# Kernel optimization log

Measured on AMD Instinct MI355X. Metric: run time of the kernel, lower is better.

The kernel has to match this reference:

```python
import jax, jax.numpy as jnp
import numpy as np

B, N, RESC, LAT, UNIT = 8, 32, 256.0, 1536, 512
CHS = [64, 64, 128, 256, 512, 512]
HS = [128, 64, 32, 16, 8, 1]


def _align(feat, P):
    # torch F.grid_sample(feat, 2*P.unsqueeze(-2)/RESC - 1, 'bilinear', 'border', align_corners=False).squeeze(-1)
    # feat: [B,C,H,W], P: [B,M,2] (x,y) pixel coords in [0,RESC); returns [B,C,M]
    Bn, C, H, W = feat.shape
    gx = 2.0 * P[..., 0] / RESC - 1.0
    gy = 2.0 * P[..., 1] / RESC - 1.0
    # align_corners=False unnormalize, then border clamp
    x = jnp.clip(((gx + 1.0) * W - 1.0) * 0.5, 0.0, W - 1.0)
    y = jnp.clip(((gy + 1.0) * H - 1.0) * 0.5, 0.0, H - 1.0)
    x0 = jnp.floor(x); y0 = jnp.floor(y)
    wx = (x - x0)[:, None, :]; wy = (y - y0)[:, None, :]
    x0i = x0.astype(jnp.int32); y0i = y0.astype(jnp.int32)
    x1i = jnp.minimum(x0i + 1, W - 1); y1i = jnp.minimum(y0i + 1, H - 1)
    flat = feat.reshape(Bn, C, H * W)
    def gat(yi, xi):
        return jnp.take_along_axis(flat, (yi * W + xi)[:, None, :], axis=2)  # [B,C,M]
    v00 = gat(y0i, x0i); v01 = gat(y0i, x1i); v10 = gat(y1i, x0i); v11 = gat(y1i, x1i)
    return v00 * (1 - wx) * (1 - wy) + v01 * wx * (1 - wy) + v10 * (1 - wx) * wy + v11 * wx * wy


def _conv1(x, w, b):
    # 1x1 Conv1d: [B,Cin,M] x [Cout,Cin] -> [B,Cout,M]
    return jnp.einsum('bci,oc->boi', x, w) + b[None, :, None]


def _rescls(x, p):
    # ResCls(n=1): intro -> (relu(BN) -> chorus, residual) -> outro ; BN in eval mode
    iw, ib, bg, bb, bm, bv, cw, cb, ow, ob = p
    x = _conv1(x, iw, ib)
    d = jax.nn.relu((x - bm[None, :, None]) * (bg / jnp.sqrt(bv + 1e-5))[None, :, None] + bb[None, :, None])
    x = x + _conv1(d, cw, cb)
    return _conv1(x, ow, ob)


def _forward(feats, P, n, gp, pp):
    # node features: concat of per-level aligned features  [B, LAT, N]
    F_ = jnp.concatenate([_align(f, P) for f in feats], axis=1)
    # edge midpoints ep[b, i*N+j] = (P[i] + P[j]) / 2  -> [B, N*N, 2]
    ep = ((P[:, :, None, :] + P[:, None, :, :]) * 0.5).reshape(B, N * N, 2)
    # L: first LAT channels = F[:, :, i], next LAT channels = F[:, :, j]
    Fi = jnp.broadcast_to(F_[:, :, :, None], (B, LAT, N, N)).reshape(B, LAT, N * N)
    Fj = jnp.broadcast_to(F_[:, :, None, :], (B, LAT, N, N)).reshape(B, LAT, N * N)
    E = jnp.concatenate([_align(f, ep) for f in feats], axis=1)  # [B, LAT, N*N]
    CE = jnp.concatenate([Fi, Fj, E], axis=1)  # [B, 3*LAT, N*N]
    gate = jax.nn.sigmoid(_rescls(CE, gp))  # [B, 1, N*N]
    pr = _rescls(CE, pp)  # [B, 64, N*N]
    pr = pr / jnp.maximum(jnp.linalg.norm(pr, axis=1, keepdims=True), 1e-12)  # F.normalize(dim=1)
    m = jnp.arange(N) < n[:, None]  # [B, N]
    mask = (m[:, None, :] & m[:, :, None]).reshape(B, 1, N * N).astype(CE.dtype)
    return (gate * pr * mask).reshape(B, 64, N, N)


def setup_inputs() -> dict:
    key = jax.random.key(0)
    ks = jax.random.split(key, 20)
    d = {}
    for i, (c, h) in enumerate(zip(CHS, HS)):
        d[f'feat{i}'] = jax.random.normal(ks[i], (B, c, h, h), jnp.float32)
    d['P'] = jax.random.uniform(ks[6], (B, N, 2), jnp.float32) * RESC
    d['n'] = jax.random.randint(ks[7], (B,), 16, N + 1, jnp.int32)
    def w(k, shape):
        return jax.random.normal(k, shape, jnp.float32) * 0.02
    for pre, cout, k0 in (('g', 1, 8), ('p', 64, 12)):
        d[pre + '_iw'] = w(ks[k0], (UNIT, 3 * LAT)); d[pre + '_ib'] = jnp.zeros((UNIT,), jnp.float32)
        d[pre + '_bg'] = jnp.ones((UNIT,), jnp.float32); d[pre + '_bb'] = jnp.zeros((UNIT,), jnp.float32)
        d[pre + '_bm'] = jnp.zeros((UNIT,), jnp.float32)
        d[pre + '_bv'] = jax.random.uniform(ks[k0 + 1], (UNIT,), jnp.float32) + 0.5
        d[pre + '_cw'] = w(ks[k0 + 2], (UNIT, UNIT)); d[pre + '_cb'] = jnp.zeros((UNIT,), jnp.float32)
        d[pre + '_ow'] = w(ks[k0 + 3], (cout, UNIT)); d[pre + '_ob'] = jnp.zeros((cout,), jnp.float32)
    return d


def reference(feat0, feat1, feat2, feat3, feat4, feat5, P, n,
              g_iw, g_ib, g_bg, g_bb, g_bm, g_bv, g_cw, g_cb, g_ow, g_ob,
              p_iw, p_ib, p_bg, p_bb, p_bm, p_bv, p_cw, p_cb, p_ow, p_ob):
    feats = (feat0, feat1, feat2, feat3, feat4, feat5)
    gp = (g_iw, g_ib, g_bg, g_bb, g_bm, g_bv, g_cw, g_cb, g_ow, g_ob)
    pp = (p_iw, p_ib, p_bg, p_bb, p_bm, p_bv, p_cw, p_cb, p_ow, p_ob)
    return _forward(feats, P, n, gp, pp)
```

## Files before the change

### kernel.cpp

```cpp
#include <hip/hip_runtime.h>
#include <hip/hip_bf16.h>

using bf16 = __hip_bfloat16;
using short8 = __attribute__((ext_vector_type(8))) short;
using f32x4  = __attribute__((ext_vector_type(4))) float;
typedef unsigned int u32;

#define LAT_ 1536

__device__ __forceinline__ void glds16(const bf16* g, bf16* l) {
  __builtin_amdgcn_global_load_lds(
      (const __attribute__((address_space(1))) void*)g,
      (__attribute__((address_space(3))) void*)l, 16, 0, 0);
}
__device__ __forceinline__ float b2f(bf16 x) { return __bfloat162float(x); }
__device__ __forceinline__ bf16 f2b(float x) { return __float2bfloat16(x); }

template<int C, int W>
__device__ __forceinline__ void trans_tile(const float* __restrict__ src, bf16* __restrict__ dst,
                                           int b, int hw0, int c0, bf16 (*tile)[72], int t) {
  constexpr int HW = W * W;
  {
    int cl = t >> 2, h0 = (t & 3) * 16;
    const float* sp = src + (long)(b * C + c0 + cl) * HW + hw0 + h0;
    #pragma unroll
    for (int k = 0; k < 16; k += 4) {
      float4 v = *(const float4*)(sp + k);
      tile[h0 + k + 0][cl] = f2b(v.x);
      tile[h0 + k + 1][cl] = f2b(v.y);
      tile[h0 + k + 2][cl] = f2b(v.z);
      tile[h0 + k + 3][cl] = f2b(v.w);
    }
  }
  __syncthreads();
  {
    int hwl = t >> 2, cc = (t & 3) * 16;
    bf16* dp = dst + ((long)b * HW + hw0 + hwl) * C + c0 + cc;
    #pragma unroll
    for (int k = 0; k < 16; k += 2) {
      __hip_bfloat162 pr;
      pr.x = tile[hwl][cc + k];
      pr.y = tile[hwl][cc + k + 1];
      *(__hip_bfloat162*)(dp + k) = pr;
    }
  }
}

__global__ __launch_bounds__(256) void prep_k(
    const float* __restrict__ g_iw, const float* __restrict__ p_iw,
    const float* __restrict__ p_cw, const float* __restrict__ p_ow, const float* __restrict__ f5,
    const float* __restrict__ g_bg, const float* __restrict__ g_bb, const float* __restrict__ g_bm,
    const float* __restrict__ g_bv, const float* __restrict__ p_bg, const float* __restrict__ p_bb,
    const float* __restrict__ p_bm, const float* __restrict__ p_bv,
    const float* __restrict__ g_ib, const float* __restrict__ p_ib, const float* __restrict__ p_cb,
    const float* __restrict__ g_ow, const float* __restrict__ g_cw,
    const float* __restrict__ g_cb, const float* __restrict__ g_ob,
    const float* __restrict__ f0, const float* __restrict__ f1, const float* __restrict__ f2,
    const float* __restrict__ f3, const float* __restrict__ f4,
    bf16* __restrict__ Wp, bf16* __restrict__ pcw16, bf16* __restrict__ pow16,
    bf16* __restrict__ T5, float* __restrict__ bnp, float* __restrict__ u,
    float* __restrict__ gacc,
    bf16* __restrict__ T0, bf16* __restrict__ T1, bf16* __restrict__ T2,
    bf16* __restrict__ T3, bf16* __restrict__ T4) {
  __shared__ bf16 tile[64][72];
  __shared__ float red[256];
  int B = blockIdx.x, t = threadIdx.x;
  if (B < 18432) {
    int seg = B / 3072;
    int idx = (B % 3072) * 256 + t;
    if (idx < 512 * 1536) {
      int r = idx / 1536, c = idx % 1536;
      const float* src; int co;
      switch (seg) {
        case 0: src = g_iw; co = 0;    break;
        case 1: src = g_iw; co = 1536; break;
        case 2: src = p_iw; co = 0;    break;
        case 3: src = p_iw; co = 1536; break;
        case 4: src = g_iw; co = 3072; break;
        default: src = p_iw; co = 3072; break;
      }
      Wp[(long)seg * 512 * 1536 + idx] = f2b(src[(long)r * 4608 + co + c]);
    }
    return;
  }
  if (B < 19456) { int idx = (B - 18432) * 256 + t; pcw16[idx] = f2b(p_cw[idx]); return; }
  if (B < 19584) { int idx = (B - 19456) * 256 + t; pow16[idx] = f2b(p_ow[idx]); return; }
  if (B < 19600) { int idx = (B - 19584) * 256 + t; T5[idx] = f2b(f5[idx]); return; }
  if (B < 19602) {
    int k = (B - 19600) * 256 + t;
    if (k < 512) {
      float sg = g_bg[k] / sqrtf(g_bv[k] + 1e-5f);
      bnp[k] = sg; bnp[512 + k] = g_bb[k] - g_bm[k] * sg;
      float sp = p_bg[k] / sqrtf(p_bv[k] + 1e-5f);
      bnp[1024 + k] = sp; bnp[1536 + k] = p_bb[k] - p_bm[k] * sp;
      bnp[2048 + k] = g_ib[k]; bnp[2560 + k] = p_ib[k];
      bnp[3584 + k] = p_cb[k];
    }
    return;
  }
  if (B < 19610) {
    __shared__ float ured[4][64];
    int k0 = (B - 19602) * 64;
    int kk = t & 63, part = t >> 6;
    int k = k0 + kk;
    float s = 0.f;
    for (int o = part * 128; o < part * 128 + 128; ++o)
      s = fmaf(g_ow[o], g_cw[o * 512 + k], s);
    ured[part][kk] = s;
    __syncthreads();
    if (part == 0) u[k] = ured[0][kk] + ured[1][kk] + ured[2][kk] + ured[3][kk];
    return;
  }
  if (B == 19610) {
    red[t] = g_ow[t] * g_cb[t] + g_ow[t + 256] * g_cb[t + 256];
    __syncthreads();
    for (int off = 128; off; off >>= 1) {
      if (t < off) red[t] += red[t + off];
      __syncthreads();
    }
    if (t == 0) bnp[3072] = red[0] + g_ob[0];
    return;
  }
  if (B < 19643) { int idx = (B - 19611) * 256 + t; gacc[idx] = 0.f; return; }
  {
    int q = B - 19643;
    int b = q / 376, tt = q % 376;
    if (tt < 256)      trans_tile<64, 128>(f0, T0, b, tt * 64, 0, tile, t);
    else if (tt < 320) trans_tile<64, 64 >(f1, T1, b, (tt - 256) * 64, 0, tile, t);
    else if (tt < 352) { int z = tt - 320; trans_tile<128, 32>(f2, T2, b, (z & 15) * 64, (z >> 4) * 64, tile, t); }
    else if (tt < 368) { int z = tt - 352; trans_tile<256, 16>(f3, T3, b, (z & 3) * 64, (z >> 2) * 64, tile, t); }
    else               { int z = tt - 368; trans_tile<512, 8 >(f4, T4, b, 0, z * 64, tile, t); }
  }
}

__device__ __forceinline__ float blo(u32 r) { return __uint_as_float(r << 16); }
__device__ __forceinline__ float bhi(u32 r) { return __uint_as_float(r & 0xffff0000u); }

template<int C, int W>
__device__ __forceinline__ void proc2(const bf16* __restrict__ T, int b,
    const float* MX, const float* MY, bf16* __restrict__ Sb, int koff, int t) {
  constexpr int C2 = C / 2, HW = W * W;
  const bf16* Tb = T + (long)b * HW * C;
  for (int idx = t; idx < 16 * C2; idx += 256) {
    int q = idx / C2, c2 = idx % C2;
    float x = MX[q], y = MY[q];
    float fx = fminf(fmaxf(x * ((float)W / 256.f) - 0.5f, 0.f), (float)(W - 1));
    float fy = fminf(fmaxf(y * ((float)W / 256.f) - 0.5f, 0.f), (float)(W - 1));
    float x0f = floorf(fx), y0f = floorf(fy);
    float wx = fx - x0f, wy = fy - y0f;
    int x0 = (int)x0f, y0 = (int)y0f;
    int x1 = min(x0 + 1, W - 1), y1 = min(y0 + 1, W - 1);
    u32 r00 = *(const u32*)&Tb[(y0 * W + x0) * C + 2 * c2];
    u32 r01 = *(const u32*)&Tb[(y0 * W + x1) * C + 2 * c2];
    u32 r10 = *(const u32*)&Tb[(y1 * W + x0) * C + 2 * c2];
    u32 r11 = *(const u32*)&Tb[(y1 * W + x1) * C + 2 * c2];
    float w00 = (1.f - wx) * (1.f - wy), w01 = wx * (1.f - wy);
    float w10 = (1.f - wx) * wy,        w11 = wx * wy;
    float vlo = blo(r00) * w00 + blo(r01) * w01 + blo(r10) * w10 + blo(r11) * w11;
    float vhi = bhi(r00) * w00 + bhi(r01) * w01 + bhi(r10) * w10 + bhi(r11) * w11;
    __hip_bfloat162 pr;
    pr.x = f2b(vlo); pr.y = f2b(vhi);
    *(__hip_bfloat162*)&Sb[(long)q * LAT_ + koff + 2 * c2] = pr;
  }
}

__global__ __launch_bounds__(256) void sample5_k(
    const bf16* __restrict__ T0, const bf16* __restrict__ T1, const bf16* __restrict__ T2,
    const bf16* __restrict__ T3, const bf16* __restrict__ T4, const bf16* __restrict__ T5,
    const float* __restrict__ P, bf16* __restrict__ Sball) {
  int b = blockIdx.z, p0 = blockIdx.x * 16, lvl = blockIdx.y, t = threadIdx.x;
  __shared__ float Px[32], Py[32], MX[16], MY[16];
  if (t < 32) { Px[t] = P[(b * 32 + t) * 2]; Py[t] = P[(b * 32 + t) * 2 + 1]; }
  __syncthreads();
  if (t < 16) {
    int m = p0 + t;
    float x, y;
    if (m < 32) { x = Px[m]; y = Py[m]; }
    else { int ij = m - 32, i = ij >> 5, j = ij & 31;
           x = 0.5f * (Px[i] + Px[j]); y = 0.5f * (Py[i] + Py[j]); }
    MX[t] = x; MY[t] = y;
  }
  __syncthreads();
  bf16* Sb = Sball + ((long)b * 1056 + p0) * LAT_;
  switch (lvl) {
    case 0: proc2<64, 128>(T0, b, MX, MY, Sb, 0,    t); break;
    case 1: proc2<64, 64 >(T1, b, MX, MY, Sb, 64,   t); break;
    case 2: proc2<128, 32>(T2, b, MX, MY, Sb, 128,  t); break;
    case 3: proc2<256, 16>(T3, b, MX, MY, Sb, 256,  t); break;
    case 4: proc2<512, 8 >(T4, b, MX, MY, Sb, 512,  t); break;
    default:
      for (int idx = t; idx < 16 * 256; idx += 256) {
        int q = idx >> 8, c2 = idx & 255;
        *(__hip_bfloat162*)&Sb[(long)q * LAT_ + 1024 + 2 * c2] =
            *(const __hip_bfloat162*)&T5[b * 512 + 2 * c2];
      }
  }
}

__global__ __launch_bounds__(256) void nodegemm_k(
    const bf16* __restrict__ Sball, const bf16* __restrict__ Wp, float* __restrict__ A4) {
  int b = blockIdx.y;
  int n0 = blockIdx.x * 64;
  int t = threadIdx.x, w = t >> 6, lane = t & 63;
  int nn = n0 + w * 16;
  int frow = lane & 15, fko = (lane >> 4) * 8;
  const bf16* Ab = Sball + (long)b * 1056 * LAT_;
  f32x4 acc[2] = {};
  for (int kb = 0; kb < LAT_; kb += 32) {
    short8 bq = *(const short8*)&Wp[(long)(nn + frow) * LAT_ + kb + fko];
    #pragma unroll
    for (int i = 0; i < 2; ++i) {
      short8 aq = *(const short8*)&Ab[(long)(i * 16 + frow) * LAT_ + kb + fko];
      acc[i] = __builtin_amdgcn_mfma_f32_16x16x32_bf16(aq, bq, acc[i], 0, 0, 0);
    }
  }
  #pragma unroll
  for (int i = 0; i < 2; ++i)
    #pragma unroll
    for (int r = 0; r < 4; ++r) {
      int m = i * 16 + (lane >> 4) * 4 + r;
      int n = nn + (lane & 15);
      A4[(long)b * 65536 + m * 2048 + n] = acc[i][r];
    }
}

__global__ __launch_bounds__(256) void edge_k(
    const bf16* __restrict__ Sball, const bf16* __restrict__ WpE,
    const float* __restrict__ bnp, const float* __restrict__ A4,
    const float* __restrict__ u, const float* __restrict__ g_ow,
    bf16* __restrict__ XFh, bf16* __restrict__ DH, float* __restrict__ gacc) {
  int b = blockIdx.z;
  int m0 = blockIdx.x * 128, n0 = blockIdx.y * 128;
  const bf16* A = Sball + (long)b * 1056 * LAT_ + 32 * LAT_;
  __shared__ bf16 Ash[128 * 32];
  __shared__ bf16 Bsh[128 * 32];
  int t = threadIdx.x, w = t >> 6, lane = t & 63;
  int mh = (w & 1) * 64, nh = (w >> 1) * 64;
  int frow = lane & 15, fko = (lane >> 4) * 8;
  int lrow = lane >> 2, lchunk = lane & 3;
  f32x4 acc[4][4] = {};
  for (int kb = 0; kb < LAT_; kb += 32) {
    #pragma unroll
    for (int q = 0; q < 2; ++q) {
      int ra = q * 64 + w * 16 + lrow;
      glds16(&A[(long)(m0 + ra) * LAT_ + kb + lchunk * 8],   &Ash[ra * 32 + lchunk * 8]);
      glds16(&WpE[(long)(n0 + ra) * LAT_ + kb + lchunk * 8], &Bsh[ra * 32 + lchunk * 8]);
    }
    __syncthreads();
    short8 af[4], bq[4];
    #pragma unroll
    for (int i = 0; i < 4; ++i) af[i] = *(const short8*)&Ash[(mh + i * 16 + frow) * 32 + fko];
    #pragma unroll
    for (int j = 0; j < 4; ++j) bq[j] = *(const short8*)&Bsh[(nh + j * 16 + frow) * 32 + fko];
    #pragma unroll
    for (int i = 0; i < 4; ++i)
      #pragma unroll
      for (int j = 0; j < 4; ++j)
        acc[i][j] = __builtin_amdgcn_mfma_f32_16x16x32_bf16(af[i], bq[j], acc[i][j], 0, 0, 0);
    __syncthreads();
  }
  if (n0 < 512) {
    float pg[16];
    #pragma unroll
    for (int z = 0; z < 16; ++z) pg[z] = 0.f;
    #pragma unroll
    for (int i = 0; i < 4; ++i) {
      #pragma unroll
      for (int j = 0; j < 4; ++j) {
        int n = n0 + nh + j * 16 + (lane & 15);
        float gw = g_ow[n], uu = u[n];
        float sc = bnp[n], sh = bnp[512 + n], ib = bnp[2048 + n];
        #pragma unroll
        for (int r = 0; r < 4; ++r) {
          int m = m0 + mh + i * 16 + (lane >> 4) * 4 + r;
          float v = acc[i][j][r] + ib
                  + A4[((long)b * 32 + (m >> 5)) * 2048 + n]
                  + A4[((long)b * 32 + (m & 31)) * 2048 + 512 + n];
          float d = fmaxf(fmaf(v, sc, sh), 0.f);
          pg[i * 4 + r] += gw * v + uu * d;
        }
      }
    }
    #pragma unroll
    for (int z = 0; z < 16; ++z) {
      float v = pg[z];
      v += __shfl_xor(v, 1, 16);
      v += __shfl_xor(v, 2, 16);
      v += __shfl_xor(v, 4, 16);
      v += __shfl_xor(v, 8, 16);
      pg[z] = v;
    }
    if ((lane & 15) == 0) {
      #pragma unroll
      for (int z = 0; z < 16; ++z) {
        int m = m0 + mh + (z >> 2) * 16 + (lane >> 4) * 4 + (z & 3);
        atomicAdd(&gacc[(long)b * 1024 + m], pg[z]);
      }
    }
  } else {
    #pragma unroll
    for (int i = 0; i < 4; ++i) {
      #pragma unroll
      for (int j = 0; j < 4; ++j) {
        int n = n0 + nh + j * 16 + (lane & 15);
        int np = n - 512;
        float sc = bnp[1024 + np], sh = bnp[1536 + np], ib = bnp[2048 + n];
        #pragma unroll
        for (int r = 0; r < 4; ++r) {
          int m = m0 + mh + i * 16 + (lane >> 4) * 4 + r;
          float v = acc[i][j][r] + ib
                  + A4[((long)b * 32 + (m >> 5)) * 2048 + 1024 + np]
                  + A4[((long)b * 32 + (m & 31)) * 2048 + 1536 + np];
          long e = ((long)b * 1024 + m) * 512 + np;
          XFh[e] = f2b(v);
          DH[e]  = f2b(fmaxf(fmaf(v, sc, sh), 0.f));
        }
      }
    }
  }
}

__global__ __launch_bounds__(256) void chorus_k(
    const bf16* __restrict__ DH, const bf16* __restrict__ pcw16,
    const float* __restrict__ bnp, const bf16* __restrict__ XFh,
    bf16* __restrict__ Yp16) {
  int b = blockIdx.z;
  int m0 = blockIdx.x * 128, n0 = blockIdx.y * 128;
  const bf16* A = DH + (long)b * 1024 * 512;
  __shared__ bf16 Ash[128 * 32];
  __shared__ bf16 Bsh[128 * 32];
  int t = threadIdx.x, w = t >> 6, lane = t & 63;
  int mh = (w & 1) * 64, nh = (w >> 1) * 64;
  int frow = lane & 15, fko = (lane >> 4) * 8;
  int lrow = lane >> 2, lchunk = lane & 3;
  f32x4 acc[4][4] = {};
  for (int kb = 0; kb < 512; kb += 32) {
    #pragma unroll
    for (int q = 0; q < 2; ++q) {
      int ra = q * 64 + w * 16 + lrow;
      glds16(&A[(long)(m0 + ra) * 512 + kb + lchunk * 8],      &Ash[ra * 32 + lchunk * 8]);
      glds16(&pcw16[(long)(n0 + ra) * 512 + kb + lchunk * 8],  &Bsh[ra * 32 + lchunk * 8]);
    }
    __syncthreads();
    short8 af[4], bq[4];
    #pragma unroll
    for (int i = 0; i < 4; ++i) af[i] = *(const short8*)&Ash[(mh + i * 16 + frow) * 32 + fko];
    #pragma unroll
    for (int j = 0; j < 4; ++j) bq[j] = *(const short8*)&Bsh[(nh + j * 16 + frow) * 32 + fko];
    #pragma unroll
    for (int i = 0; i < 4; ++i)
      #pragma unroll
      for (int j = 0; j < 4; ++j)
        acc[i][j] = __builtin_amdgcn_mfma_f32_16x16x32_bf16(af[i], bq[j], acc[i][j], 0, 0, 0);
    __syncthreads();
  }
  #pragma unroll
  for (int i = 0; i < 4; ++i)
    #pragma unroll
    for (int j = 0; j < 4; ++j)
      #pragma unroll
      for (int r = 0; r < 4; ++r) {
        int m = m0 + mh + i * 16 + (lane >> 4) * 4 + r;
        int n = n0 + nh + j * 16 + (lane & 15);
        float v = acc[i][j][r] + bnp[3584 + n]
                + b2f(XFh[((long)b * 1024 + m) * 512 + n]);
        Yp16[((long)b * 1024 + m) * 512 + n] = f2b(v);
      }
}

__global__ __launch_bounds__(256) void ofinal_k(
    const bf16* __restrict__ Yp16, const bf16* __restrict__ pow16,
    const float* __restrict__ p_ob, const float* __restrict__ gacc,
    const float* __restrict__ bnp, const int* __restrict__ nvec,
    float* __restrict__ out) {
  int b = blockIdx.y;
  int m0 = blockIdx.x * 64;
  const bf16* Ab = Yp16 + (long)b * 1024 * 512;
  __shared__ bf16 Ash[64][40];
  __shared__ bf16 Bsh[64][40];
  __shared__ float ol[64][65];
  int t = threadIdx.x, w = t >> 6, lane = t & 63;
  int mq = w * 16;
  int frow = lane & 15, fko = (lane >> 4) * 8;
  f32x4 acc[4] = {};
  for (int kb = 0; kb < 512; kb += 32) {
    { int r = t >> 2, ko = (t & 3) * 8;
      *(uint4*)&Ash[r][ko] = *(const uint4*)&Ab[(long)(m0 + r) * 512 + kb + ko];
      *(uint4*)&Bsh[r][ko] = *(const uint4*)&pow16[(long)r * 512 + kb + ko]; }
    __syncthreads();
    short8 af = *(const short8*)&Ash[mq + frow][fko];
    #pragma unroll
    for (int j = 0; j < 4; ++j) {
      short8 bq = *(const short8*)&Bsh[j * 16 + frow][fko];
      acc[j] = __builtin_amdgcn_mfma_f32_16x16x32_bf16(af, bq, acc[j], 0, 0, 0);
    }
    __syncthreads();
  }
  float pr[4][4], ssl[4] = {0.f, 0.f, 0.f, 0.f};
  #pragma unroll
  for (int j = 0; j < 4; ++j) {
    float bias = p_ob[j * 16 + (lane & 15)];
    #pragma unroll
    for (int r = 0; r < 4; ++r) {
      float v = acc[j][r] + bias;
      pr[j][r] = v;
      ssl[r] = fmaf(v, v, ssl[r]);
    }
  }
  #pragma unroll
  for (int r = 0; r < 4; ++r) {
    float v = ssl[r];
    v += __shfl_xor(v, 1, 16);
    v += __shfl_xor(v, 2, 16);
    v += __shfl_xor(v, 4, 16);
    v += __shfl_xor(v, 8, 16);
    ssl[r] = v;
  }
  int nb = nvec[b];
  float gconst = bnp[3072];
  float scale[4];
  #pragma unroll
  for (int r = 0; r < 4; ++r) {
    int m = m0 + mq + (lane >> 4) * 4 + r;
    float gl = gacc[(long)b * 1024 + m] + gconst;
    float gate = 1.f / (1.f + expf(-gl));
    int ii = m >> 5, jj = m & 31;
    float maskv = (ii < nb && jj < nb) ? 1.f : 0.f;
    scale[r] = gate * maskv / fmaxf(sqrtf(ssl[r]), 1e-12f);
  }
  #pragma unroll
  for (int j = 0; j < 4; ++j)
    #pragma unroll
    for (int r = 0; r < 4; ++r)
      ol[mq + (lane >> 4) * 4 + r][j * 16 + (lane & 15)] = pr[j][r] * scale[r];
  __syncthreads();
  {
    int c = t >> 2, ms = (t & 3) * 16;
    float* op = out + ((long)b * 64 + c) * 1024 + m0 + ms;
    #pragma unroll
    for (int k = 0; k < 16; k += 4) {
      float4 v;
      v.x = ol[ms + k + 0][c];
      v.y = ol[ms + k + 1][c];
      v.z = ol[ms + k + 2][c];
      v.w = ol[ms + k + 3][c];
      *(float4*)(op + k) = v;
    }
  }
}

extern "C" void kernel_launch(void* const* d_in, const int* in_sizes, int n_in,
                              void* d_out, int out_size, void* d_ws, size_t ws_size,
                              hipStream_t stream) {
  const float* f0 = (const float*)d_in[0];
  const float* f1 = (const float*)d_in[1];
  const float* f2 = (const float*)d_in[2];
  const float* f3 = (const float*)d_in[3];
  const float* f4 = (const float*)d_in[4];
  const float* f5 = (const float*)d_in[5];
  const float* P  = (const float*)d_in[6];
  const int*   n  = (const int*)d_in[7];
  const float *g_iw=(const float*)d_in[8],  *g_ib=(const float*)d_in[9],
              *g_bg=(const float*)d_in[10], *g_bb=(const float*)d_in[11],
              *g_bm=(const float*)d_in[12], *g_bv=(const float*)d_in[13],
              *g_cw=(const float*)d_in[14], *g_cb=(const float*)d_in[15],
              *g_ow=(const float*)d_in[16], *g_ob=(const float*)d_in[17];
  const float *p_iw=(const float*)d_in[18], *p_ib=(const float*)d_in[19],
              *p_bg=(const float*)d_in[20], *p_bb=(const float*)d_in[21],
              *p_bm=(const float*)d_in[22], *p_bv=(const float*)d_in[23],
              *p_cw=(const float*)d_in[24], *p_cb=(const float*)d_in[25],
              *p_ow=(const float*)d_in[26], *p_ob=(const float*)d_in[27];
  float* out = (float*)d_out;
  char* wsb = (char*)d_ws;

  bf16*  Sb    = (bf16*)(wsb + 0);
  bf16*  Wp    = (bf16*)(wsb + 25952256);
  bf16*  pcw16 = (bf16*)(wsb + 35389440);
  bf16*  pow16 = (bf16*)(wsb + 35913728);
  bf16*  T5    = (bf16*)(wsb + 35979264);
  float* bnp   = (float*)(wsb + 35987456);
  float* u     = (float*)(wsb + 36003840);
  float* gacc  = (float*)(wsb + 36005888);
  float* A4    = (float*)(wsb + 36038656);
  bf16*  XFh   = (bf16*)(wsb + 38135808);
  bf16*  DH    = (bf16*)(wsb + 46524416);
  bf16*  Yp16  = (bf16*)(wsb + 54913024);
  bf16*  T0 = (bf16*)(wsb + 38135808);
  bf16*  T1 = (bf16*)(wsb + 54913024);
  bf16*  T2 = (bf16*)(wsb + 59107328);
  bf16*  T3 = (bf16*)(wsb + 61204480);
  bf16*  T4 = (bf16*)(wsb + 62253056);
  bf16*  WpE = Wp + (long)2048 * LAT_;

  prep_k<<<22651, 256, 0, stream>>>(g_iw, p_iw, p_cw, p_ow, f5,
      g_bg, g_bb, g_bm, g_bv, p_bg, p_bb, p_bm, p_bv, g_ib, p_ib, p_cb,
      g_ow, g_cw, g_cb, g_ob, f0, f1, f2, f3, f4,
      Wp, pcw16, pow16, T5, bnp, u, gacc, T0, T1, T2, T3, T4);
  sample5_k<<<dim3(66, 6, 8), 256, 0, stream>>>(T0, T1, T2, T3, T4, T5, P, Sb);
  nodegemm_k<<<dim3(32, 8), 256, 0, stream>>>(Sb, Wp, A4);
  edge_k<<<dim3(8, 8, 8), 256, 0, stream>>>(Sb, WpE, bnp, A4, u, g_ow, XFh, DH, gacc);
  chorus_k<<<dim3(8, 4, 8), 256, 0, stream>>>(DH, pcw16, bnp, XFh, Yp16);
  ofinal_k<<<dim3(16, 8), 256, 0, stream>>>(Yp16, pow16, p_ob, gacc, bnp, n, out);
}
```

Measured before the change: 256.8 us.

## Fold chorus conv into output conv and merge tail kernels into one

Precomputes V = p_ow·p_cw and a folded bias in the prep kernel. This lets the final output be computed as XF·p_owᵀ + DH·Vᵀ in one fused post kernel, replacing the separate 512-wide chorus GEMM and the output GEMM, along with their bf16 intermediate round-trip. The node GEMM is also restructured so each block loops over all 8 batches while reusing the weight fragment, which leaves 32 blocks instead of 256. The risks are bf16 rounding of the folded V, a naive serial 512-length dot product per element in prep, and reduced parallelism in the node GEMM.

```diff
diff --git a/kernel.cpp b/kernel.cpp
--- a/kernel.cpp
+++ b/kernel.cpp
@@ -53,11 +53,12 @@
     const float* __restrict__ g_bv, const float* __restrict__ p_bg, const float* __restrict__ p_bb,
     const float* __restrict__ p_bm, const float* __restrict__ p_bv,
     const float* __restrict__ g_ib, const float* __restrict__ p_ib, const float* __restrict__ p_cb,
+    const float* __restrict__ p_ob,
     const float* __restrict__ g_ow, const float* __restrict__ g_cw,
     const float* __restrict__ g_cb, const float* __restrict__ g_ob,
     const float* __restrict__ f0, const float* __restrict__ f1, const float* __restrict__ f2,
     const float* __restrict__ f3, const float* __restrict__ f4,
-    bf16* __restrict__ Wp, bf16* __restrict__ pcw16, bf16* __restrict__ pow16,
+    bf16* __restrict__ Wp, bf16* __restrict__ pow16, bf16* __restrict__ V16,
     bf16* __restrict__ T5, float* __restrict__ bnp, float* __restrict__ u,
     float* __restrict__ gacc,
     bf16* __restrict__ T0, bf16* __restrict__ T1, bf16* __restrict__ T2,
@@ -83,24 +84,22 @@
     }
     return;
   }
-  if (B < 19456) { int idx = (B - 18432) * 256 + t; pcw16[idx] = f2b(p_cw[idx]); return; }
-  if (B < 19584) { int idx = (B - 19456) * 256 + t; pow16[idx] = f2b(p_ow[idx]); return; }
-  if (B < 19600) { int idx = (B - 19584) * 256 + t; T5[idx] = f2b(f5[idx]); return; }
-  if (B < 19602) {
-    int k = (B - 19600) * 256 + t;
+  if (B < 18560) { int idx = (B - 18432) * 256 + t; pow16[idx] = f2b(p_ow[idx]); return; }
+  if (B < 18576) { int idx = (B - 18560) * 256 + t; T5[idx] = f2b(f5[idx]); return; }
+  if (B < 18578) {
+    int k = (B - 18576) * 256 + t;
     if (k < 512) {
       float sg = g_bg[k] / sqrtf(g_bv[k] + 1e-5f);
       bnp[k] = sg; bnp[512 + k] = g_bb[k] - g_bm[k] * sg;
       float sp = p_bg[k] / sqrtf(p_bv[k] + 1e-5f);
       bnp[1024 + k] = sp; bnp[1536 + k] = p_bb[k] - p_bm[k] * sp;
       bnp[2048 + k] = g_ib[k]; bnp[2560 + k] = p_ib[k];
-      bnp[3584 + k] = p_cb[k];
     }
     return;
   }
-  if (B < 19610) {
+  if (B < 18586) {
     __shared__ float ured[4][64];
-    int k0 = (B - 19602) * 64;
+    int k0 = (B - 18578) * 64;
     int kk = t & 63, part = t >> 6;
     int k = k0 + kk;
     float s = 0.f;
@@ -111,7 +110,7 @@
     if (part == 0) u[k] = ured[0][kk] + ured[1][kk] + ured[2][kk] + ured[3][kk];
     return;
   }
-  if (B == 19610) {
+  if (B == 18586) {
     red[t] = g_ow[t] * g_cb[t] + g_ow[t + 256] * g_cb[t + 256];
     __syncthreads();
     for (int off = 128; off; off >>= 1) {
@@ -121,9 +120,26 @@
     if (t == 0) bnp[3072] = red[0] + g_ob[0];
     return;
   }
-  if (B < 19643) { int idx = (B - 19611) * 256 + t; gacc[idx] = 0.f; return; }
+  if (B < 18619) { int idx = (B - 18587) * 256 + t; gacc[idx] = 0.f; return; }
+  if (B < 18747) {
+    int idx = (B - 18619) * 256 + t;
+    int c = idx >> 9, k = idx & 511;
+    float s = 0.f;
+    for (int nn = 0; nn < 512; ++nn)
+      s = fmaf(p_ow[c * 512 + nn], p_cw[nn * 512 + k], s);
+    V16[idx] = f2b(s);
+    return;
+  }
+  if (B == 18747) {
+    if (t < 64) {
+      float s = p_ob[t];
+      for (int nn = 0; nn < 512; ++nn) s = fmaf(p_ow[t * 512 + nn], p_cb[nn], s);
+      bnp[3104 + t] = s;
+    }
+    return;
+  }
   {
-    int q = B - 19643;
+    int q = B - 18748;
     int b = q / 376, tt = q % 376;
     if (tt < 256)      trans_tile<64, 128>(f0, T0, b, tt * 64, 0, tile, t);
     else if (tt < 320) trans_tile<64, 64 >(f1, T1, b, (tt - 256) * 64, 0, tile, t);
@@ -199,29 +215,33 @@
 
 __global__ __launch_bounds__(256) void nodegemm_k(
     const bf16* __restrict__ Sball, const bf16* __restrict__ Wp, float* __restrict__ A4) {
-  int b = blockIdx.y;
   int n0 = blockIdx.x * 64;
   int t = threadIdx.x, w = t >> 6, lane = t & 63;
   int nn = n0 + w * 16;
   int frow = lane & 15, fko = (lane >> 4) * 8;
-  const bf16* Ab = Sball + (long)b * 1056 * LAT_;
-  f32x4 acc[2] = {};
+  f32x4 acc[8][2] = {};
   for (int kb = 0; kb < LAT_; kb += 32) {
     short8 bq = *(const short8*)&Wp[(long)(nn + frow) * LAT_ + kb + fko];
     #pragma unroll
-    for (int i = 0; i < 2; ++i) {
-      short8 aq = *(const short8*)&Ab[(long)(i * 16 + frow) * LAT_ + kb + fko];
-      acc[i] = __builtin_amdgcn_mfma_f32_16x16x32_bf16(aq, bq, acc[i], 0, 0, 0);
+    for (int b = 0; b < 8; ++b) {
+      const bf16* Ab = Sball + (long)b * 1056 * LAT_;
+      #pragma unroll
+      for (int i = 0; i < 2; ++i) {
+        short8 aq = *(const short8*)&Ab[(long)(i * 16 + frow) * LAT_ + kb + fko];
+        acc[b][i] = __builtin_amdgcn_mfma_f32_16x16x32_bf16(aq, bq, acc[b][i], 0, 0, 0);
+      }
     }
   }
   #pragma unroll
-  for (int i = 0; i < 2; ++i)
-    #pragma unroll
-    for (int r = 0; r < 4; ++r) {
-      int m = i * 16 + (lane >> 4) * 4 + r;
-      int n = nn + (lane & 15);
-      A4[(long)b * 65536 + m * 2048 + n] = acc[i][r];
-    }
+  for (int b = 0; b < 8; ++b)
+    #pragma unroll
+    for (int i = 0; i < 2; ++i)
+      #pragma unroll
+      for (int r = 0; r < 4; ++r) {
+        int m = i * 16 + (lane >> 4) * 4 + r;
+        int n = nn + (lane & 15);
+        A4[(long)b * 65536 + m * 2048 + n] = acc[b][i][r];
+      }
 }
 
 __global__ __launch_bounds__(256) void edge_k(
@@ -320,125 +340,114 @@
   }
 }
 
-__global__ __launch_bounds__(256) void chorus_k(
-    const bf16* __restrict__ DH, const bf16* __restrict__ pcw16,
-    const float* __restrict__ bnp, const bf16* __restrict__ XFh,
-    bf16* __restrict__ Yp16) {
-  int b = blockIdx.z;
-  int m0 = blockIdx.x * 128, n0 = blockIdx.y * 128;
-  const bf16* A = DH + (long)b * 1024 * 512;
-  __shared__ bf16 Ash[128 * 32];
-  __shared__ bf16 Bsh[128 * 32];
+__global__ __launch_bounds__(256) void post_k(
+    const bf16* __restrict__ XFh, const bf16* __restrict__ DH,
+    const bf16* __restrict__ pow16, const bf16* __restrict__ V16,
+    const float* __restrict__ bnp, const float* __restrict__ gacc,
+    const int* __restrict__ nvec, float* __restrict__ out) {
+  int b = blockIdx.y;
+  int m0 = blockIdx.x * 128;
+  __shared__ float smem_f[128 * 65];
+  bf16* Xsh = (bf16*)smem_f;
+  bf16* Dsh = Xsh + 4096;
+  bf16* Psh = Xsh + 8192;
+  bf16* Vsh = Xsh + 10240;
+  float (*ol)[65] = (float(*)[65])smem_f;
   int t = threadIdx.x, w = t >> 6, lane = t & 63;
-  int mh = (w & 1) * 64, nh = (w >> 1) * 64;
+  int mh = w * 32;
   int frow = lane & 15, fko = (lane >> 4) * 8;
   int lrow = lane >> 2, lchunk = lane & 3;
-  f32x4 acc[4][4] = {};
+  const bf16* Xa = XFh + (long)b * 1024 * 512;
+  const bf16* Da = DH + (long)b * 1024 * 512;
+  f32x4 acc[2][4] = {};
   for (int kb = 0; kb < 512; kb += 32) {
     #pragma unroll
     for (int q = 0; q < 2; ++q) {
-      int ra = q * 64 + w * 16 + lrow;
-      glds16(&A[(long)(m0 + ra) * 512 + kb + lchunk * 8],      &Ash[ra * 32 + lchunk * 8]);
-      glds16(&pcw16[(long)(n0 + ra) * 512 + kb + lchunk * 8],  &Bsh[ra * 32 + lchunk * 8]);
+      int ra = mh + q * 16 + lrow;
+      glds16(&Xa[(long)(m0 + ra) * 512 + kb + lchunk * 8], &Xsh[ra * 32 + lchunk * 8]);
+      glds16(&Da[(long)(m0 + ra) * 512 + kb + lchunk * 8], &Dsh[ra * 32 + lchunk * 8]);
+    }
+    {
+      int rb = w * 16 + lrow;
+      glds16(&pow16[(long)rb * 512 + kb + lchunk * 8], &Psh[rb * 32 + lchunk * 8]);
+      glds16(&V16[(long)rb * 512 + kb + lchunk * 8],   &Vsh[rb * 32 + lchunk * 8]);
     }
     __syncthreads();
-    short8 af[4], bq[4];
-    #pragma unroll
-    for (int i = 0; i < 4; ++i) af[i] = *(const short8*)&Ash[(mh + i * 16 + frow) * 32 + fko];
-    #pragma unroll
-    for (int j = 0; j < 4; ++j) bq[j] = *(const short8*)&Bsh[(nh + j * 16 + frow) * 32 + fko];
-    #pragma unroll
-    for (int i = 0; i < 4; ++i)
-      #pragma unroll
-      for (int j = 0; j < 4; ++j)
-        acc[i][j] = __builtin_amdgcn_mfma_f32_16x16x32_bf16(af[i], bq[j], acc[i][j], 0, 0, 0);
+    short8 ax[2], ad[2], bp[4], bv[4];
+    #pragma unroll
+    for (int i = 0; i < 2; ++i) {
+      ax[i] = *(const short8*)&Xsh[(mh + i * 16 + frow) * 32 + fko];
+      ad[i] = *(const short8*)&Dsh[(mh + i * 16 + frow) * 32 + fko];
+    }
+    #pragma unroll
+    for (int j = 0; j < 4; ++j) {
+      bp[j] = *(const short8*)&Psh[(j * 16 + frow) * 32 + fko];
+      bv[j] = *(const short8*)&Vsh[(j * 16 + frow) * 32 + fko];
+    }
+    #pragma unroll
+    for (int i = 0; i < 2; ++i)
+      #pragma unroll
+      for (int j = 0; j < 4; ++j) {
+        acc[i][j] = __builtin_amdgcn_mfma_f32_16x16x32_bf16(ax[i], bp[j], acc[i][j], 0, 0, 0);
+        acc[i][j] = __builtin_amdgcn_mfma_f32_16x16x32_bf16(ad[i], bv[j], acc[i][j], 0, 0, 0);
+      }
     __syncthreads();
   }
+  float val[2][4][4], ssl[2][4];
   #pragma unroll
-  for (int i = 0; i < 4; ++i)
-    #pragma unroll
-    for (int j = 0; j < 4; ++j)
+  for (int i = 0; i < 2; ++i)
+    #pragma unroll
+    for (int r = 0; r < 4; ++r) ssl[i][r] = 0.f;
+  #pragma unroll
+  for (int i = 0; i < 2; ++i)
+    #pragma unroll
+    for (int j = 0; j < 4; ++j) {
+      float pc = bnp[3104 + j * 16 + (lane & 15)];
       #pragma unroll
       for (int r = 0; r < 4; ++r) {
-        int m = m0 + mh + i * 16 + (lane >> 4) * 4 + r;
-        int n = n0 + nh + j * 16 + (lane & 15);
-        float v = acc[i][j][r] + bnp[3584 + n]
-                + b2f(XFh[((long)b * 1024 + m) * 512 + n]);
-        Yp16[((long)b * 1024 + m) * 512 + n] = f2b(v);
-      }
-}
-
-__global__ __launch_bounds__(256) void ofinal_k(
-    const bf16* __restrict__ Yp16, const bf16* __restrict__ pow16,
-    const float* __restrict__ p_ob, const float* __restrict__ gacc,
-    const float* __restrict__ bnp, const int* __restrict__ nvec,
-    float* __restrict__ out) {
-  int b = blockIdx.y;
-  int m0 = blockIdx.x * 64;
-  const bf16* Ab = Yp16 + (long)b * 1024 * 512;
-  __shared__ bf16 Ash[64][40];
-  __shared__ bf16 Bsh[64][40];
-  __shared__ float ol[64][65];
-  int t = threadIdx.x, w = t >> 6, lane = t & 63;
-  int mq = w * 16;
-  int frow = lane & 15, fko = (lane >> 4) * 8;
-  f32x4 acc[4] = {};
-  for (int kb = 0; kb < 512; kb += 32) {
-    { int r = t >> 2, ko = (t & 3) * 8;
-      *(uint4*)&Ash[r][ko] = *(const uint4*)&Ab[(long)(m0 + r) * 512 + kb + ko];
-      *(uint4*)&Bsh[r][ko] = *(const uint4*)&pow16[(long)r * 512 + kb + ko]; }
-    __syncthreads();
-    short8 af = *(const short8*)&Ash[mq + frow][fko];
-    #pragma unroll
-    for (int j = 0; j < 4; ++j) {
-      short8 bq = *(const short8*)&Bsh[j * 16 + frow][fko];
-      acc[j] = __builtin_amdgcn_mfma_f32_16x16x32_bf16(af, bq, acc[j], 0, 0, 0);
-    }
-    __syncthreads();
-  }
-  float pr[4][4], ssl[4] = {0.f, 0.f, 0.f, 0.f};
+        float v = acc[i][j][r] + pc;
+        val[i][j][r] = v;
+        ssl[i][r] = fmaf(v, v, ssl[i][r]);
+      }
+    }
   #pragma unroll
-  for (int j = 0; j < 4; ++j) {
-    float bias = p_ob[j * 16 + (lane & 15)];
+  for (int i = 0; i < 2; ++i)
     #pragma unroll
     for (int r = 0; r < 4; ++r) {
-      float v = acc[j][r] + bias;
-      pr[j][r] = v;
-      ssl[r] = fmaf(v, v, ssl[r]);
-    }
-  }
-  #pragma unroll
-  for (int r = 0; r < 4; ++r) {
-    float v = ssl[r];
-    v += __shfl_xor(v, 1, 16);
-    v += __shfl_xor(v, 2, 16);
-    v += __shfl_xor(v, 4, 16);
-    v += __shfl_xor(v, 8, 16);
-    ssl[r] = v;
-  }
+      float v = ssl[i][r];
+      v += __shfl_xor(v, 1, 16);
+      v += __shfl_xor(v, 2, 16);
+      v += __shfl_xor(v, 4, 16);
+      v += __shfl_xor(v, 8, 16);
+      ssl[i][r] = v;
+    }
   int nb = nvec[b];
   float gconst = bnp[3072];
-  float scale[4];
+  float scale[2][4];
   #pragma unroll
-  for (int r = 0; r < 4; ++r) {
-    int m = m0 + mq + (lane >> 4) * 4 + r;
-    float gl = gacc[(long)b * 1024 + m] + gconst;
-    float gate = 1.f / (1.f + expf(-gl));
-    int ii = m >> 5, jj = m & 31;
-    float maskv = (ii < nb && jj < nb) ? 1.f : 0.f;
-    scale[r] = gate * maskv / fmaxf(sqrtf(ssl[r]), 1e-12f);
-  }
+  for (int i = 0; i < 2; ++i)
+    #pragma unroll
+    for (int r = 0; r < 4; ++r) {
+      int m = m0 + mh + i * 16 + (lane >> 4) * 4 + r;
+      float gl = gacc[(long)b * 1024 + m] + gconst;
+      float gate = 1.f / (1.f + expf(-gl));
+      int ii = m >> 5, jj = m & 31;
+      float maskv = (ii < nb && jj < nb) ? 1.f : 0.f;
+      scale[i][r] = gate * maskv / fmaxf(sqrtf(ssl[i][r]), 1e-12f);
+    }
   #pragma unroll
-  for (int j = 0; j < 4; ++j)
-    #pragma unroll
-    for (int r = 0; r < 4; ++r)
-      ol[mq + (lane >> 4) * 4 + r][j * 16 + (lane & 15)] = pr[j][r] * scale[r];
+  for (int i = 0; i < 2; ++i)
+    #pragma unroll
+    for (int j = 0; j < 4; ++j)
+      #pragma unroll
+      for (int r = 0; r < 4; ++r)
+        ol[mh + i * 16 + (lane >> 4) * 4 + r][j * 16 + (lane & 15)] = val[i][j][r] * scale[i][r];
   __syncthreads();
   {
-    int c = t >> 2, ms = (t & 3) * 16;
+    int c = t >> 2, ms = (t & 3) * 32;
     float* op = out + ((long)b * 64 + c) * 1024 + m0 + ms;
     #pragma unroll
-    for (int k = 0; k < 16; k += 4) {
+    for (int k = 0; k < 32; k += 4) {
       float4 v;
       v.x = ol[ms + k + 0][c];
       v.y = ol[ms + k + 1][c];
@@ -475,30 +484,28 @@
 
   bf16*  Sb    = (bf16*)(wsb + 0);
   bf16*  Wp    = (bf16*)(wsb + 25952256);
-  bf16*  pcw16 = (bf16*)(wsb + 35389440);
-  bf16*  pow16 = (bf16*)(wsb + 35913728);
-  bf16*  T5    = (bf16*)(wsb + 35979264);
-  float* bnp   = (float*)(wsb + 35987456);
-  float* u     = (float*)(wsb + 36003840);
-  float* gacc  = (float*)(wsb + 36005888);
-  float* A4    = (float*)(wsb + 36038656);
-  bf16*  XFh   = (bf16*)(wsb + 38135808);
-  bf16*  DH    = (bf16*)(wsb + 46524416);
-  bf16*  Yp16  = (bf16*)(wsb + 54913024);
-  bf16*  T0 = (bf16*)(wsb + 38135808);
-  bf16*  T1 = (bf16*)(wsb + 54913024);
-  bf16*  T2 = (bf16*)(wsb + 59107328);
-  bf16*  T3 = (bf16*)(wsb + 61204480);
-  bf16*  T4 = (bf16*)(wsb + 62253056);
+  bf16*  pow16 = (bf16*)(wsb + 35389440);
+  bf16*  V16   = (bf16*)(wsb + 35454976);
+  bf16*  T5    = (bf16*)(wsb + 35520512);
+  float* bnp   = (float*)(wsb + 35528704);
+  float* u     = (float*)(wsb + 35545088);
+  float* gacc  = (float*)(wsb + 35547136);
+  float* A4    = (float*)(wsb + 35579904);
+  bf16*  XFh   = (bf16*)(wsb + 37677056);
+  bf16*  DH    = (bf16*)(wsb + 46065664);
+  bf16*  T0 = (bf16*)(wsb + 37677056);
+  bf16*  T1 = (bf16*)(wsb + 54454272);
+  bf16*  T2 = (bf16*)(wsb + 58648576);
+  bf16*  T3 = (bf16*)(wsb + 60745728);
+  bf16*  T4 = (bf16*)(wsb + 61794304);
   bf16*  WpE = Wp + (long)2048 * LAT_;
 
-  prep_k<<<22651, 256, 0, stream>>>(g_iw, p_iw, p_cw, p_ow, f5,
-      g_bg, g_bb, g_bm, g_bv, p_bg, p_bb, p_bm, p_bv, g_ib, p_ib, p_cb,
+  prep_k<<<21756, 256, 0, stream>>>(g_iw, p_iw, p_cw, p_ow, f5,
+      g_bg, g_bb, g_bm, g_bv, p_bg, p_bb, p_bm, p_bv, g_ib, p_ib, p_cb, p_ob,
       g_ow, g_cw, g_cb, g_ob, f0, f1, f2, f3, f4,
-      Wp, pcw16, pow16, T5, bnp, u, gacc, T0, T1, T2, T3, T4);
+      Wp, pow16, V16, T5, bnp, u, gacc, T0, T1, T2, T3, T4);
   sample5_k<<<dim3(66, 6, 8), 256, 0, stream>>>(T0, T1, T2, T3, T4, T5, P, Sb);
-  nodegemm_k<<<dim3(32, 8), 256, 0, stream>>>(Sb, Wp, A4);
+  nodegemm_k<<<32, 256, 0, stream>>>(Sb, Wp, A4);
   edge_k<<<dim3(8, 8, 8), 256, 0, stream>>>(Sb, WpE, bnp, A4, u, g_ow, XFh, DH, gacc);
-  chorus_k<<<dim3(8, 4, 8), 256, 0, stream>>>(DH, pcw16, bnp, XFh, Yp16);
-  ofinal_k<<<dim3(16, 8), 256, 0, stream>>>(Yp16, pow16, p_ob, gacc, bnp, n, out);
-}
+  post_k<<<dim3(8, 8), 256, 0, stream>>>(XFh, DH, pow16, V16, bnp, gacc, n, out);
+}
```

After: 412.6 us. 1.61x slower.
